# Kernel tuning notes

Measured on AMD Instinct MI355X. Metric: run time of the kernel, lower is better.

Reference implementation:

```python
import jax, jax.numpy as jnp
import numpy as np

EPS = 1e-12  # torch F.normalize eps
NUM_HEADS = 4
DT = 0.25
NUM_STEPS = 4


def _l2norm(x, axis=-1):
    n = jnp.sqrt(jnp.sum(x * x, axis=axis, keepdims=True))
    return x / jnp.maximum(n, EPS)


def setup_inputs() -> dict:
    key = jax.random.key(0)
    k0, k1, k2, k3, k4 = jax.random.split(key, 5)
    B, T, D = 4, 2048, 256
    z = jax.random.normal(k0, (B, T, D), dtype=jnp.float32)
    omega = jax.random.normal(k1, (1, 1, D), dtype=jnp.float32) * 0.1
    Wqk = jax.random.normal(k2, (2 * D, D), dtype=jnp.float32) * (1.0 / np.sqrt(D))
    Wout = jax.random.normal(k3, (D, D), dtype=jnp.float32) * (1.0 / np.sqrt(D))
    bout = jax.random.normal(k4, (D,), dtype=jnp.float32) * 0.01
    return {"z": z, "omega": omega, "Wqk": Wqk, "Wout": Wout, "bout": bout}


def _kuramoto(x, omega, Wqk, Wout, bout):
    # x: [B, T, D]
    B, T, D = x.shape
    hd = D // NUM_HEADS
    qk = x @ Wqk.T  # [B, T, 2D]
    q, k = jnp.split(qk, 2, axis=-1)
    q = _l2norm(q.reshape(B, T, NUM_HEADS, hd))  # cosine-normalized per head
    k = _l2norm(k.reshape(B, T, NUM_HEADS, hd))
    # coupling: [B, H, T, T] cosine similarity
    coupling = jnp.einsum("bqhd,bkhd->bhqk", q, k)
    # sin nonlinearity replaces softmax
    force = jnp.einsum("bhqk,bkhd->bqhd", jnp.sin(coupling), k).reshape(B, T, D)
    return omega + force @ Wout.T + bout


def reference(z, omega, Wqk, Wout, bout):
    def f(x):
        return _kuramoto(x, omega, Wqk, Wout, bout)

    x = z
    for _ in range(NUM_STEPS):
        x = _l2norm(x)
        k1 = f(x)
        k2 = f(x + DT / 2 * k1)
        k3 = f(x + DT / 2 * k2)
        k4 = f(x + DT * k3)
        x = x + DT / 6 * (k1 + 2 * k2 + 2 * k3 + k4)
    return _l2norm(x)
```

## Files before the change

kernel.cpp:

```cpp
#include <hip/hip_runtime.h>
#include <cmath>

#define NB 4
#define TT 2048
#define DD 256
#define NH 4
#define BT (NB*TT)

static constexpr float DT_ = 0.25f;

typedef _Float16 f16x8 __attribute__((ext_vector_type(8)));
typedef _Float16 f16x4 __attribute__((ext_vector_type(4)));
typedef float    f32x4 __attribute__((ext_vector_type(4)));

static constexpr size_t HSZ = (size_t)NB * NH * TT * 64;
static constexpr size_t FSZ = (size_t)BT * 256;

__global__ __launch_bounds__(256)
void split_weights(const float* __restrict__ Wqk, const float* __restrict__ Wout,
                   _Float16* __restrict__ WqkH, _Float16* __restrict__ WqkL,
                   _Float16* __restrict__ WoutH, _Float16* __restrict__ WoutL)
{
    const int idx = blockIdx.x * 256 + threadIdx.x;
    const float4 v = (idx < 32768) ? ((const float4*)Wqk)[idx]
                                   : ((const float4*)Wout)[idx - 32768];
    f16x4 h, l;
    h[0]=(_Float16)v.x; l[0]=(_Float16)(v.x-(float)h[0]);
    h[1]=(_Float16)v.y; l[1]=(_Float16)(v.y-(float)h[1]);
    h[2]=(_Float16)v.z; l[2]=(_Float16)(v.z-(float)h[2]);
    h[3]=(_Float16)v.w; l[3]=(_Float16)(v.w-(float)h[3]);
    if (idx < 32768) { ((f16x4*)WqkH)[idx] = h; ((f16x4*)WqkL)[idx] = l; }
    else { ((f16x4*)WoutH)[idx-32768] = h; ((f16x4*)WoutL)[idx-32768] = l; }
}

__global__ __launch_bounds__(256)
void comb_weights(const float* __restrict__ Wqk, const float* __restrict__ Wout,
                  const float* __restrict__ omega, const float* __restrict__ bout,
                  _Float16* __restrict__ WcombH, _Float16* __restrict__ WcombL,
                  float* __restrict__ qkob)
{
    __shared__ float qrow[256];
    __shared__ float pr[256];
    const int n = blockIdx.x;
    const int k = threadIdx.x;
    qrow[k] = Wqk[n * 256 + k];
    __syncthreads();
    float s = 0.f;
    for (int m = 0; m < 256; ++m) s = fmaf(qrow[m], Wout[m * 256 + k], s);
    const _Float16 h = (_Float16)s;
    WcombH[n * 256 + k] = h;
    WcombL[n * 256 + k] = (_Float16)(s - (float)h);
    pr[k] = (omega[k] + bout[k]) * qrow[k];
    __syncthreads();
    if (k == 0) {
        float t = 0.f;
        for (int i = 0; i < 256; ++i) t += pr[i];
        qkob[n] = t;
    }
}

__global__ __launch_bounds__(256)
void l2norm_rows(const float* __restrict__ src, float* __restrict__ dst,
                 _Float16* __restrict__ dstH, _Float16* __restrict__ dstL) {
    const int wave = threadIdx.x >> 6;
    const int lane = threadIdx.x & 63;
    const size_t row = (size_t)blockIdx.x * 4 + wave;
    float4 v = ((const float4*)(src + row * DD))[lane];
    float ss = v.x*v.x + v.y*v.y + v.z*v.z + v.w*v.w;
    #pragma unroll
    for (int off = 32; off; off >>= 1) ss += __shfl_xor(ss, off, 64);
    const float inv = 1.0f / fmaxf(sqrtf(ss), 1e-12f);
    v.x *= inv; v.y *= inv; v.z *= inv; v.w *= inv;
    ((float4*)(dst + row * DD))[lane] = v;
    if (dstH != nullptr) {
        f16x4 h, l;
        h[0]=(_Float16)v.x; l[0]=(_Float16)(v.x-(float)h[0]);
        h[1]=(_Float16)v.y; l[1]=(_Float16)(v.y-(float)h[1]);
        h[2]=(_Float16)v.z; l[2]=(_Float16)(v.z-(float)h[2]);
        h[3]=(_Float16)v.w; l[3]=(_Float16)(v.w-(float)h[3]);
        ((f16x4*)(dstH + row * DD))[lane] = h;
        ((f16x4*)(dstL + row * DD))[lane] = l;
    }
}

__global__ __launch_bounds__(256)
void reduce_F(const float* __restrict__ Fp, float* __restrict__ Facc,
              _Float16* __restrict__ SH, _Float16* __restrict__ SL, int faccm)
{
    const size_t idx = (size_t)blockIdx.x * 256 + threadIdx.x;
    const float4 a = ((const float4*)Fp)[idx];
    const float4 b = ((const float4*)(Fp + FSZ))[idx];
    const float4 c = ((const float4*)(Fp + 2*FSZ))[idx];
    float4 s = make_float4(a.x+b.x+c.x, a.y+b.y+c.y, a.z+b.z+c.z, a.w+b.w+c.w);
    if (faccm == 1) {
        ((float4*)Facc)[idx] = s;
    } else if (faccm == 2) {
        float4 f = ((const float4*)Facc)[idx];
        f.x += 2.f*s.x; f.y += 2.f*s.y; f.z += 2.f*s.z; f.w += 2.f*s.w;
        ((float4*)Facc)[idx] = f;
    } else {
        const float4 f = ((const float4*)Facc)[idx];
        s.x += f.x; s.y += f.y; s.z += f.z; s.w += f.w;
    }
    f16x4 h, l;
    h[0]=(_Float16)s.x; l[0]=(_Float16)(s.x-(float)h[0]);
    h[1]=(_Float16)s.y; l[1]=(_Float16)(s.y-(float)h[1]);
    h[2]=(_Float16)s.z; l[2]=(_Float16)(s.z-(float)h[2]);
    h[3]=(_Float16)s.w; l[3]=(_Float16)(s.w-(float)h[3]);
    ((f16x4*)SH)[idx] = h;
    ((f16x4*)SL)[idx] = l;
}

__global__ __launch_bounds__(256, 3)
void gemm_mfma(const _Float16* __restrict__ AH, const _Float16* __restrict__ AL,
               const _Float16* __restrict__ BH, const _Float16* __restrict__ BL,
               float* __restrict__ qkx, const float* __restrict__ qkob,
               const float* __restrict__ omega, const float* __restrict__ bout,
               const float* __restrict__ xin, float* __restrict__ xout,
               _Float16* __restrict__ Qhi, _Float16* __restrict__ Qlo,
               _Float16* __restrict__ Khi, _Float16* __restrict__ Klo,
               _Float16* __restrict__ KtrH,
               int mode, float cc)
{
    __shared__ _Float16 Ah[128 * 64];
    __shared__ _Float16 Al[128 * 64];
    __shared__ _Float16 Bh[64 * 64];
    __shared__ _Float16 Bl[64 * 64];
    const int m0 = blockIdx.x * 128, n0 = blockIdx.y * 64;
    const int t  = threadIdx.x;
    const int w  = t >> 6;
    const int l  = t & 63;
    const int lr = l & 15;
    const int lq = l >> 4;

    f32x4 acc[2][4];
    #pragma unroll
    for (int s = 0; s < 2; ++s)
        #pragma unroll
        for (int nt = 0; nt < 4; ++nt) acc[s][nt] = (f32x4){0.f,0.f,0.f,0.f};

    int rdo[8];
    #pragma unroll
    for (int ch = 0; ch < 8; ++ch) rdo[ch] = ((ch ^ (lr & 7)) * 8);

    for (int kc = 0; kc < 4; ++kc) {
        const int k0 = kc * 64;
        __syncthreads();
        #pragma unroll
        for (int s2 = 0; s2 < 4; ++s2) {
            const int idx = t + 256 * s2;
            const int r = idx >> 3, lc = idx & 7;
            const int sw = ((lc ^ (r & 7)) * 8);
            *(uint4*)&Ah[r * 64 + sw] = *(const uint4*)(AH + (size_t)(m0 + r) * 256 + k0 + lc * 8);
            *(uint4*)&Al[r * 64 + sw] = *(const uint4*)(AL + (size_t)(m0 + r) * 256 + k0 + lc * 8);
        }
        #pragma unroll
        for (int s2 = 0; s2 < 2; ++s2) {
            const int idx = t + 256 * s2;
            const int r = idx >> 3, lc = idx & 7;
            const int sw = ((lc ^ (r & 7)) * 8);
            *(uint4*)&Bh[r * 64 + sw] = *(const uint4*)(BH + (size_t)(n0 + r) * 256 + k0 + lc * 8);
            *(uint4*)&Bl[r * 64 + sw] = *(const uint4*)(BL + (size_t)(n0 + r) * 256 + k0 + lc * 8);
        }
        __syncthreads();
        #pragma unroll
        for (int c = 0; c < 2; ++c) {
            const int xo = rdo[4*c + lq];
            f16x8 ah[2], al[2], bh[4], bl[4];
            #pragma unroll
            for (int s = 0; s < 2; ++s) {
                ah[s] = *(const f16x8*)&Ah[(32*w + 16*s + lr) * 64 + xo];
                al[s] = *(const f16x8*)&Al[(32*w + 16*s + lr) * 64 + xo];
            }
            #pragma unroll
            for (int nt = 0; nt < 4; ++nt) {
                bh[nt] = *(const f16x8*)&Bh[(16*nt + lr) * 64 + xo];
                bl[nt] = *(const f16x8*)&Bl[(16*nt + lr) * 64 + xo];
            }
            #pragma unroll
            for (int s = 0; s < 2; ++s)
                #pragma unroll
                for (int nt = 0; nt < 4; ++nt) {
                    acc[s][nt] = __builtin_amdgcn_mfma_f32_16x16x32_f16(ah[s], bh[nt], acc[s][nt], 0, 0, 0);
                    acc[s][nt] = __builtin_amdgcn_mfma_f32_16x16x32_f16(ah[s], bl[nt], acc[s][nt], 0, 0, 0);
                    acc[s][nt] = __builtin_amdgcn_mfma_f32_16x16x32_f16(al[s], bh[nt], acc[s][nt], 0, 0, 0);
                }
        }
    }

    if (mode == 2) {
        #pragma unroll
        for (int s = 0; s < 2; ++s) {
            const int row0 = m0 + 32*w + 16*s + 4*lq;
            #pragma unroll
            for (int nt = 0; nt < 4; ++nt) {
                const int col = n0 + 16*nt + lr;
                const float ob = omega[col] + bout[col];
                #pragma unroll
                for (int r = 0; r < 4; ++r) {
                    const size_t off = (size_t)(row0 + r) * 256 + col;
                    xout[off] = xin[off] + (DT_ / 6.0f) * acc[s][nt][r] + DT_ * ob;
                }
            }
        }
    } else {
        float val[2][4][4];
        #pragma unroll
        for (int s = 0; s < 2; ++s) {
            const int row0 = m0 + 32*w + 16*s + 4*lq;
            #pragma unroll
            for (int nt = 0; nt < 4; ++nt) {
                const int col = n0 + 16*nt + lr;
                #pragma unroll
                for (int r = 0; r < 4; ++r) {
                    const size_t qo = (size_t)(row0 + r) * 512 + col;
                    if (mode == 0) {
                        val[s][nt][r] = acc[s][nt][r];
                        qkx[qo] = acc[s][nt][r];
                    } else {
                        val[s][nt][r] = qkx[qo] + cc * (acc[s][nt][r] + qkob[col]);
                    }
                }
            }
        }
        float ss[2][4];
        #pragma unroll
        for (int s = 0; s < 2; ++s)
            #pragma unroll
            for (int r = 0; r < 4; ++r) {
                float v = 0.f;
                #pragma unroll
                for (int nt = 0; nt < 4; ++nt) v += val[s][nt][r] * val[s][nt][r];
                ss[s][r] = v;
            }
        #pragma unroll
        for (int off = 1; off < 16; off <<= 1)
            #pragma unroll
            for (int s = 0; s < 2; ++s)
                #pragma unroll
                for (int r = 0; r < 4; ++r)
                    ss[s][r] += __shfl_xor(ss[s][r], off, 64);
        const int  b    = m0 >> 11;
        const int  h    = (n0 >> 6) & 3;
        const bool is_k = (n0 >= 256);
        const size_t bhi = (size_t)b * NH + h;
        _Float16* dhi = (is_k ? Khi : Qhi) + bhi * (size_t)TT * 64;
        _Float16* dlo = (is_k ? Klo : Qlo) + bhi * (size_t)TT * 64;
        const int mloc = m0 & (TT - 1);
        #pragma unroll
        for (int s = 0; s < 2; ++s) {
            const int r0 = 32*w + 16*s + 4*lq;
            float inv[4];
            #pragma unroll
            for (int r = 0; r < 4; ++r) inv[r] = 1.0f / fmaxf(sqrtf(ss[s][r]), 1e-12f);
            #pragma unroll
            for (int nt = 0; nt < 4; ++nt) {
                const int d = 16*nt + lr;
                f16x4 hv, lv;
                #pragma unroll
                for (int r = 0; r < 4; ++r) {
                    const float v2 = val[s][nt][r] * inv[r];
                    hv[r] = (_Float16)v2;
                    lv[r] = (_Float16)(v2 - (float)hv[r]);
                    dhi[(size_t)(mloc + r0 + r) * 64 + d] = hv[r];
                    dlo[(size_t)(mloc + r0 + r) * 64 + d] = lv[r];
                }
                if (is_k) {
                    const size_t tb = bhi * (size_t)64 * TT + (size_t)d * TT + mloc + r0;
                    *(f16x4*)(KtrH + tb) = hv;
                }
            }
        }
    }
}

__global__ __launch_bounds__(256, 3)
void kuramoto_attn(const _Float16* __restrict__ Qhi, const _Float16* __restrict__ Qlo,
                   const _Float16* __restrict__ Khi, const _Float16* __restrict__ Klo,
                   const _Float16* __restrict__ KtrH,
                   float* __restrict__ Fp)
{
    __shared__ _Float16 KjH[64 * 64];
    __shared__ _Float16 KjL[64 * 64];
    __shared__ _Float16 KdH[64 * 64];
    __shared__ _Float16 Pw[4][2][16 * 68];
    const int bh = blockIdx.z;
    const int b  = bh >> 2, h = bh & 3;
    const size_t base  = (size_t)bh * TT * 64;
    const size_t tbase = (size_t)bh * 64 * TT;
    const int t0 = blockIdx.y * 11;
    const int tn = (blockIdx.y == 2) ? 10 : 11;
    float* Fout = Fp + (size_t)blockIdx.y * FSZ;
    const int t = threadIdx.x;
    const int w = t >> 6;
    const int l = t & 63;
    const int lr = l & 15;
    const int lq = l >> 4;
    const int i0 = blockIdx.x * 128 + w * 32;

    f16x8 qh[2][2], ql[2][2];
    #pragma unroll
    for (int s = 0; s < 2; ++s) {
        const size_t qoff = base + (size_t)(i0 + 16*s + lr) * 64 + lq * 8;
        qh[s][0] = *(const f16x8*)(Qhi + qoff);
        qh[s][1] = *(const f16x8*)(Qhi + qoff + 32);
        ql[s][0] = *(const f16x8*)(Qlo + qoff);
        ql[s][1] = *(const f16x8*)(Qlo + qoff + 32);
    }

    f32x4 Facc[2][4];
    #pragma unroll
    for (int s = 0; s < 2; ++s)
        #pragma unroll
        for (int nt = 0; nt < 4; ++nt) Facc[s][nt] = (f32x4){0.f, 0.f, 0.f, 0.f};

    const int sr = t >> 3;
    const int lc = t & 7;
    const int so = lc * 8;
    const int sw = ((lc ^ (sr & 7)) * 8);
    const int x0 = ((lq     ^ (lr & 7)) * 8);
    const int x1 = (((lq+4) ^ (lr & 7)) * 8);

    for (int tt = 0; tt < tn; ++tt) {
        const int j0 = (t0 + tt) * 64;
        __syncthreads();
        {
            *(uint4*)&KjH[sr * 64 + sw]        = *(const uint4*)(Khi + base + (size_t)(j0 + sr) * 64 + so);
            *(uint4*)&KjH[(sr + 32) * 64 + sw] = *(const uint4*)(Khi + base + (size_t)(j0 + sr + 32) * 64 + so);
            *(uint4*)&KjL[sr * 64 + sw]        = *(const uint4*)(Klo + base + (size_t)(j0 + sr) * 64 + so);
            *(uint4*)&KjL[(sr + 32) * 64 + sw] = *(const uint4*)(Klo + base + (size_t)(j0 + sr + 32) * 64 + so);
            *(uint4*)&KdH[sr * 64 + sw]        = *(const uint4*)(KtrH + tbase + (size_t)sr * TT + j0 + so);
            *(uint4*)&KdH[(sr + 32) * 64 + sw] = *(const uint4*)(KtrH + tbase + (size_t)(sr + 32) * TT + j0 + so);
        }
        __syncthreads();
        #pragma unroll
        for (int nt = 0; nt < 4; ++nt) {
            f16x8 kh0 = *(const f16x8*)&KjH[(16*nt + lr) * 64 + x0];
            f16x8 kh1 = *(const f16x8*)&KjH[(16*nt + lr) * 64 + x1];
            f16x8 kl0 = *(const f16x8*)&KjL[(16*nt + lr) * 64 + x0];
            f16x8 kl1 = *(const f16x8*)&KjL[(16*nt + lr) * 64 + x1];
            #pragma unroll
            for (int s = 0; s < 2; ++s) {
                f32x4 a = (f32x4){0.f, 0.f, 0.f, 0.f};
                a = __builtin_amdgcn_mfma_f32_16x16x32_f16(kh0, qh[s][0], a, 0, 0, 0);
                a = __builtin_amdgcn_mfma_f32_16x16x32_f16(kh1, qh[s][1], a, 0, 0, 0);
                a = __builtin_amdgcn_mfma_f32_16x16x32_f16(kl0, qh[s][0], a, 0, 0, 0);
                a = __builtin_amdgcn_mfma_f32_16x16x32_f16(kl1, qh[s][1], a, 0, 0, 0);
                a = __builtin_amdgcn_mfma_f32_16x16x32_f16(kh0, ql[s][0], a, 0, 0, 0);
                a = __builtin_amdgcn_mfma_f32_16x16x32_f16(kh1, ql[s][1], a, 0, 0, 0);
                f16x4 pv;
                #pragma unroll
                for (int r = 0; r < 4; ++r) pv[r] = (_Float16)__sinf(a[r]);
                *(f16x4*)&Pw[w][s][lr * 68 + 16*nt + 4*lq] = pv;
            }
        }
        f16x8 ph[2][2];
        #pragma unroll
        for (int s = 0; s < 2; ++s) {
            ph[s][0] = *(const f16x8*)&Pw[w][s][lr * 68 + lq * 8];
            ph[s][1] = *(const f16x8*)&Pw[w][s][lr * 68 + 32 + lq * 8];
        }
        #pragma unroll
        for (int nt = 0; nt < 4; ++nt) {
            f16x8 kh0 = *(const f16x8*)&KdH[(16*nt + lr) * 64 + x0];
            f16x8 kh1 = *(const f16x8*)&KdH[(16*nt + lr) * 64 + x1];
            #pragma unroll
            for (int s = 0; s < 2; ++s) {
                Facc[s][nt] = __builtin_amdgcn_mfma_f32_16x16x32_f16(ph[s][0], kh0, Facc[s][nt], 0, 0, 0);
                Facc[s][nt] = __builtin_amdgcn_mfma_f32_16x16x32_f16(ph[s][1], kh1, Facc[s][nt], 0, 0, 0);
            }
        }
    }
    #pragma unroll
    for (int s = 0; s < 2; ++s) {
        float* fo = Fout + ((size_t)b * TT + i0 + 16*s + 4*lq) * 256 + h * 64 + lr;
        #pragma unroll
        for (int nt = 0; nt < 4; ++nt)
            #pragma unroll
            for (int r = 0; r < 4; ++r)
                fo[(size_t)r * 256 + nt * 16] = Facc[s][nt][r];
    }
}

extern "C" void kernel_launch(void* const* d_in, const int* in_sizes, int n_in,
                              void* d_out, int out_size, void* d_ws, size_t ws_size,
                              hipStream_t stream) {
    const float* z     = (const float*)d_in[0];
    const float* omega = (const float*)d_in[1];
    const float* Wqk   = (const float*)d_in[2];
    const float* Wout  = (const float*)d_in[3];
    const float* bout  = (const float*)d_in[4];

    float* x    = (float*)d_ws;
    float* Facc = x + FSZ;
    float* Fp   = Facc + FSZ;
    float* qkx  = Fp + 3 * FSZ;
    float* qkob = qkx + (size_t)BT * 512;
    _Float16* xsH  = (_Float16*)(qkob + 512);
    _Float16* xsL  = xsH  + FSZ;
    _Float16* Qhi  = xsL  + FSZ;
    _Float16* Qlo  = Qhi  + HSZ;
    _Float16* Khi  = Qlo  + HSZ;
    _Float16* Klo  = Khi  + HSZ;
    _Float16* KtrH = Klo  + HSZ;
    _Float16* WqkH = KtrH + HSZ;
    _Float16* WqkL = WqkH + (size_t)512 * 256;
    _Float16* WoutH= WqkL + (size_t)512 * 256;
    _Float16* WoutL= WoutH + (size_t)256 * 256;
    _Float16* WcombH = WoutL + (size_t)256 * 256;
    _Float16* WcombL = WcombH + (size_t)512 * 256;

    split_weights<<<192, 256, 0, stream>>>(Wqk, Wout, WqkH, WqkL, WoutH, WoutL);
    comb_weights<<<512, 256, 0, stream>>>(Wqk, Wout, omega, bout, WcombH, WcombL, qkob);

    for (int step = 0; step < 4; ++step) {
        l2norm_rows<<<BT / 4, 256, 0, stream>>>(step == 0 ? z : x, x, xsH, xsL);
        gemm_mfma<<<dim3(BT / 128, 8), 256, 0, stream>>>(
            xsH, xsL, WqkH, WqkL, qkx, nullptr,
            nullptr, nullptr, nullptr, nullptr,
            Qhi, Qlo, Khi, Klo, KtrH, 0, 0.f);
        kuramoto_attn<<<dim3(TT / 128, 3, NB * NH), 256, 0, stream>>>(
            Qhi, Qlo, Khi, Klo, KtrH, Fp);
        for (int s = 1; s <= 3; ++s) {
            const float cs = (s == 3) ? 0.25f : 0.125f;
            reduce_F<<<2048, 256, 0, stream>>>(Fp, Facc, xsH, xsL, (s == 1) ? 1 : 2);
            gemm_mfma<<<dim3(BT / 128, 8), 256, 0, stream>>>(
                xsH, xsL, WcombH, WcombL, qkx, qkob,
                nullptr, nullptr, nullptr, nullptr,
                Qhi, Qlo, Khi, Klo, KtrH, 1, cs);
            kuramoto_attn<<<dim3(TT / 128, 3, NB * NH), 256, 0, stream>>>(
                Qhi, Qlo, Khi, Klo, KtrH, Fp);
        }
        reduce_F<<<2048, 256, 0, stream>>>(Fp, Facc, xsH, xsL, 3);
        gemm_mfma<<<dim3(BT / 128, 4), 256, 0, stream>>>(
            xsH, xsL, WoutH, WoutL, nullptr, nullptr,
            omega, bout, x, x,
            nullptr, nullptr, nullptr, nullptr, nullptr, 2, 0.f);
    }
    l2norm_rows<<<BT / 4, 256, 0, stream>>>(x, (float*)d_out, nullptr, nullptr);
}
```

Before: 1.287 ms.

## Use direct global-to-LDS loads, swizzle P tile, raise occupancy and MFMA priority

Replaces register-staged global-to-shared copies in both the projection GEMM and the attention kernel with global_load_lds DMA-style loads, pre-swizzling the global source column so the XOR-swizzled LDS layout is preserved. The padded P scratch tile becomes an unpadded XOR-swizzled layout, which cuts LDS use. Occupancy for the attention kernel goes from 3 to 4 blocks per CU, and s_setprio is wrapped around the MFMA chains. This aims to remove VGPR round-trips and LDS bank conflicts, but risks register spills at the higher occupancy bound.

```diff
diff --git a/kernel.cpp b/kernel.cpp
--- a/kernel.cpp
+++ b/kernel.cpp
@@ -15,6 +15,13 @@
 
 static constexpr size_t HSZ = (size_t)NB * NH * TT * 64;
 static constexpr size_t FSZ = (size_t)BT * 256;
+
+__device__ __forceinline__ void gload16(const void* g, void* l) {
+    __builtin_amdgcn_global_load_lds(
+        (const __attribute__((address_space(1))) void*)g,
+        (__attribute__((address_space(3))) void*)l,
+        16, 0, 0);
+}
 
 __global__ __launch_bounds__(256)
 void split_weights(const float* __restrict__ Wqk, const float* __restrict__ Wout,
@@ -132,6 +139,9 @@
     const int l  = t & 63;
     const int lr = l & 15;
     const int lq = l >> 4;
+    const int m7 = lr & 7;
+    const int rr = l >> 3;
+    const int cg = ((l & 7) ^ rr) * 8;
 
     f32x4 acc[2][4];
     #pragma unroll
@@ -139,43 +149,33 @@
         #pragma unroll
         for (int nt = 0; nt < 4; ++nt) acc[s][nt] = (f32x4){0.f,0.f,0.f,0.f};
 
-    int rdo[8];
-    #pragma unroll
-    for (int ch = 0; ch < 8; ++ch) rdo[ch] = ((ch ^ (lr & 7)) * 8);
-
     for (int kc = 0; kc < 4; ++kc) {
         const int k0 = kc * 64;
         __syncthreads();
         #pragma unroll
-        for (int s2 = 0; s2 < 4; ++s2) {
-            const int idx = t + 256 * s2;
-            const int r = idx >> 3, lc = idx & 7;
-            const int sw = ((lc ^ (r & 7)) * 8);
-            *(uint4*)&Ah[r * 64 + sw] = *(const uint4*)(AH + (size_t)(m0 + r) * 256 + k0 + lc * 8);
-            *(uint4*)&Al[r * 64 + sw] = *(const uint4*)(AL + (size_t)(m0 + r) * 256 + k0 + lc * 8);
-        }
-        #pragma unroll
-        for (int s2 = 0; s2 < 2; ++s2) {
-            const int idx = t + 256 * s2;
-            const int r = idx >> 3, lc = idx & 7;
-            const int sw = ((lc ^ (r & 7)) * 8);
-            *(uint4*)&Bh[r * 64 + sw] = *(const uint4*)(BH + (size_t)(n0 + r) * 256 + k0 + lc * 8);
-            *(uint4*)&Bl[r * 64 + sw] = *(const uint4*)(BL + (size_t)(n0 + r) * 256 + k0 + lc * 8);
+        for (int a = 0; a < 4; ++a) {
+            const int rg = 8*w + 32*a;
+            gload16(AH + (size_t)(m0 + rg + rr) * 256 + k0 + cg, &Ah[rg * 64]);
+            gload16(AL + (size_t)(m0 + rg + rr) * 256 + k0 + cg, &Al[rg * 64]);
+            if (a < 2) {
+                gload16(BH + (size_t)(n0 + rg + rr) * 256 + k0 + cg, &Bh[rg * 64]);
+                gload16(BL + (size_t)(n0 + rg + rr) * 256 + k0 + cg, &Bl[rg * 64]);
+            }
         }
         __syncthreads();
         #pragma unroll
         for (int c = 0; c < 2; ++c) {
-            const int xo = rdo[4*c + lq];
+            const int xo = (((4*c + lq) ^ m7) << 4);
             f16x8 ah[2], al[2], bh[4], bl[4];
             #pragma unroll
             for (int s = 0; s < 2; ++s) {
-                ah[s] = *(const f16x8*)&Ah[(32*w + 16*s + lr) * 64 + xo];
-                al[s] = *(const f16x8*)&Al[(32*w + 16*s + lr) * 64 + xo];
+                ah[s] = *(const f16x8*)((const char*)Ah + (32*w + 16*s + lr) * 128 + xo);
+                al[s] = *(const f16x8*)((const char*)Al + (32*w + 16*s + lr) * 128 + xo);
             }
             #pragma unroll
             for (int nt = 0; nt < 4; ++nt) {
-                bh[nt] = *(const f16x8*)&Bh[(16*nt + lr) * 64 + xo];
-                bl[nt] = *(const f16x8*)&Bl[(16*nt + lr) * 64 + xo];
+                bh[nt] = *(const f16x8*)((const char*)Bh + (16*nt + lr) * 128 + xo);
+                bl[nt] = *(const f16x8*)((const char*)Bl + (16*nt + lr) * 128 + xo);
             }
             #pragma unroll
             for (int s = 0; s < 2; ++s)
@@ -274,7 +274,7 @@
     }
 }
 
-__global__ __launch_bounds__(256, 3)
+__global__ __launch_bounds__(256, 4)
 void kuramoto_attn(const _Float16* __restrict__ Qhi, const _Float16* __restrict__ Qlo,
                    const _Float16* __restrict__ Khi, const _Float16* __restrict__ Klo,
                    const _Float16* __restrict__ KtrH,
@@ -283,7 +283,7 @@
     __shared__ _Float16 KjH[64 * 64];
     __shared__ _Float16 KjL[64 * 64];
     __shared__ _Float16 KdH[64 * 64];
-    __shared__ _Float16 Pw[4][2][16 * 68];
+    __shared__ _Float16 Pw[4][2][16 * 64];
     const int bh = blockIdx.z;
     const int b  = bh >> 2, h = bh & 3;
     const size_t base  = (size_t)bh * TT * 64;
@@ -297,6 +297,18 @@
     const int lr = l & 15;
     const int lq = l >> 4;
     const int i0 = blockIdx.x * 128 + w * 32;
+    const int m7 = lr & 7;
+    const int x0 = ((lq ^ m7) << 4);
+    const int x1 = (((lq + 4) ^ m7) << 4);
+    const int rr = l >> 3;
+    const int cg = ((l & 7) ^ rr) * 8;
+
+    const _Float16* gKh = Khi  + base  + (size_t)(8*w + rr) * 64 + cg;
+    const _Float16* gKl = Klo  + base  + (size_t)(8*w + rr) * 64 + cg;
+    const _Float16* gKd = KtrH + tbase + (size_t)(8*w + rr) * TT + cg;
+    _Float16* lKh = &KjH[(8*w) * 64];
+    _Float16* lKl = &KjL[(8*w) * 64];
+    _Float16* lKd = &KdH[(8*w) * 64];
 
     f16x8 qh[2][2], ql[2][2];
     #pragma unroll
@@ -314,61 +326,59 @@
         #pragma unroll
         for (int nt = 0; nt < 4; ++nt) Facc[s][nt] = (f32x4){0.f, 0.f, 0.f, 0.f};
 
-    const int sr = t >> 3;
-    const int lc = t & 7;
-    const int so = lc * 8;
-    const int sw = ((lc ^ (sr & 7)) * 8);
-    const int x0 = ((lq     ^ (lr & 7)) * 8);
-    const int x1 = (((lq+4) ^ (lr & 7)) * 8);
-
     for (int tt = 0; tt < tn; ++tt) {
         const int j0 = (t0 + tt) * 64;
         __syncthreads();
-        {
-            *(uint4*)&KjH[sr * 64 + sw]        = *(const uint4*)(Khi + base + (size_t)(j0 + sr) * 64 + so);
-            *(uint4*)&KjH[(sr + 32) * 64 + sw] = *(const uint4*)(Khi + base + (size_t)(j0 + sr + 32) * 64 + so);
-            *(uint4*)&KjL[sr * 64 + sw]        = *(const uint4*)(Klo + base + (size_t)(j0 + sr) * 64 + so);
-            *(uint4*)&KjL[(sr + 32) * 64 + sw] = *(const uint4*)(Klo + base + (size_t)(j0 + sr + 32) * 64 + so);
-            *(uint4*)&KdH[sr * 64 + sw]        = *(const uint4*)(KtrH + tbase + (size_t)sr * TT + j0 + so);
-            *(uint4*)&KdH[(sr + 32) * 64 + sw] = *(const uint4*)(KtrH + tbase + (size_t)(sr + 32) * TT + j0 + so);
-        }
+        gload16(gKh + (size_t)j0 * 64,           lKh);
+        gload16(gKh + (size_t)j0 * 64 + 32 * 64, lKh + 32 * 64);
+        gload16(gKl + (size_t)j0 * 64,           lKl);
+        gload16(gKl + (size_t)j0 * 64 + 32 * 64, lKl + 32 * 64);
+        gload16(gKd + j0,                        lKd);
+        gload16(gKd + j0 + (size_t)32 * TT,      lKd + 32 * 64);
         __syncthreads();
         #pragma unroll
         for (int nt = 0; nt < 4; ++nt) {
-            f16x8 kh0 = *(const f16x8*)&KjH[(16*nt + lr) * 64 + x0];
-            f16x8 kh1 = *(const f16x8*)&KjH[(16*nt + lr) * 64 + x1];
-            f16x8 kl0 = *(const f16x8*)&KjL[(16*nt + lr) * 64 + x0];
-            f16x8 kl1 = *(const f16x8*)&KjL[(16*nt + lr) * 64 + x1];
+            const int rb = (16*nt + lr) * 128;
+            f16x8 kh0 = *(const f16x8*)((const char*)KjH + rb + x0);
+            f16x8 kh1 = *(const f16x8*)((const char*)KjH + rb + x1);
+            f16x8 kl0 = *(const f16x8*)((const char*)KjL + rb + x0);
+            f16x8 kl1 = *(const f16x8*)((const char*)KjL + rb + x1);
             #pragma unroll
             for (int s = 0; s < 2; ++s) {
                 f32x4 a = (f32x4){0.f, 0.f, 0.f, 0.f};
+                __builtin_amdgcn_s_setprio(1);
                 a = __builtin_amdgcn_mfma_f32_16x16x32_f16(kh0, qh[s][0], a, 0, 0, 0);
                 a = __builtin_amdgcn_mfma_f32_16x16x32_f16(kh1, qh[s][1], a, 0, 0, 0);
                 a = __builtin_amdgcn_mfma_f32_16x16x32_f16(kl0, qh[s][0], a, 0, 0, 0);
                 a = __builtin_amdgcn_mfma_f32_16x16x32_f16(kl1, qh[s][1], a, 0, 0, 0);
                 a = __builtin_amdgcn_mfma_f32_16x16x32_f16(kh0, ql[s][0], a, 0, 0, 0);
                 a = __builtin_amdgcn_mfma_f32_16x16x32_f16(kh1, ql[s][1], a, 0, 0, 0);
+                __builtin_amdgcn_s_setprio(0);
                 f16x4 pv;
                 #pragma unroll
                 for (int r = 0; r < 4; ++r) pv[r] = (_Float16)__sinf(a[r]);
-                *(f16x4*)&Pw[w][s][lr * 68 + 16*nt + 4*lq] = pv;
+                *(f16x4*)((char*)&Pw[w][s][0] + lr * 128
+                          + (((2*nt + (lq >> 1)) ^ m7) << 4) + ((lq & 1) << 3)) = pv;
             }
         }
         f16x8 ph[2][2];
         #pragma unroll
         for (int s = 0; s < 2; ++s) {
-            ph[s][0] = *(const f16x8*)&Pw[w][s][lr * 68 + lq * 8];
-            ph[s][1] = *(const f16x8*)&Pw[w][s][lr * 68 + 32 + lq * 8];
+            ph[s][0] = *(const f16x8*)((const char*)&Pw[w][s][0] + lr * 128 + x0);
+            ph[s][1] = *(const f16x8*)((const char*)&Pw[w][s][0] + lr * 128 + x1);
         }
         #pragma unroll
         for (int nt = 0; nt < 4; ++nt) {
-            f16x8 kh0 = *(const f16x8*)&KdH[(16*nt + lr) * 64 + x0];
-            f16x8 kh1 = *(const f16x8*)&KdH[(16*nt + lr) * 64 + x1];
+            const int rb = (16*nt + lr) * 128;
+            f16x8 kh0 = *(const f16x8*)((const char*)KdH + rb + x0);
+            f16x8 kh1 = *(const f16x8*)((const char*)KdH + rb + x1);
+            __builtin_amdgcn_s_setprio(1);
             #pragma unroll
             for (int s = 0; s < 2; ++s) {
                 Facc[s][nt] = __builtin_amdgcn_mfma_f32_16x16x32_f16(ph[s][0], kh0, Facc[s][nt], 0, 0, 0);
                 Facc[s][nt] = __builtin_amdgcn_mfma_f32_16x16x32_f16(ph[s][1], kh1, Facc[s][nt], 0, 0, 0);
             }
+            __builtin_amdgcn_s_setprio(0);
         }
     }
     #pragma unroll
```

Measured after the change: 1.164 ms. 1.11x faster.
